# Kernel optimization log

Hardware: AMD Instinct MI355X
Metric: run time of the kernel (lower is better)

The kernel has to match this reference:

```python
import jax, jax.numpy as jnp
import numpy as np

# Hyperparameters (from init_kwargs)
B, N, K = 4, 16384, 16          # batch, points, kNN neighbors
C_IN, C_OUT = 64, 128           # in_planes, out_planes
KSIZE, DIL, STRIDE = 9, 1, 1    # WeightedConv1D kernel
PAD = DIL * (KSIZE // 2)        # padding = dilation*(k//2)
SIGMA = 0.02
NEG_SLOPE = 0.2                 # leakyrelu default in DeepGCN BasicConv
EPS = 1e-5                      # BatchNorm eps


def setup_inputs() -> dict:
    key = jax.random.key(0)
    ks = jax.random.split(key, 6)
    x = jax.random.normal(ks[0], (B, C_IN, N), jnp.float32)
    coords = jax.random.uniform(ks[1], (B, 3, N), jnp.float32)
    edge_index = jax.random.randint(ks[2], (2, B, N, K), 0, N)
    # EdgeConv MLP: Conv2d(2*C_IN, C_IN, 1, bias=False) -> BN -> LeakyReLU
    w_edge = jax.random.normal(ks[3], (C_IN, 2 * C_IN), jnp.float32) * (1.0 / np.sqrt(2 * C_IN))
    bn_gamma = jnp.ones((C_IN,), jnp.float32)
    bn_beta = jnp.zeros((C_IN,), jnp.float32)
    # WeightedConv1D learned kernel [C_out, C_in, k] + bias
    w_conv = jax.random.normal(ks[4], (C_OUT, C_IN, KSIZE), jnp.float32) * (1.0 / np.sqrt(C_IN * KSIZE))
    b_conv = jnp.zeros((C_OUT,), jnp.float32)
    return dict(x=x, coords=coords, edge_index=edge_index, w_edge=w_edge,
                bn_gamma=bn_gamma, bn_beta=bn_beta, w_conv=w_conv, b_conv=b_conv)


def _edge_conv(x, edge_index, w_edge, gamma, beta):
    # x: [B, C, N]; edge_index: [2, B, N, K]
    x_t = jnp.transpose(x, (0, 2, 1))                        # [B, N, C]
    gather = jax.vmap(lambda xt, idx: xt[idx])               # ([N,C],[N,K]) -> [N,K,C]
    x_j = gather(x_t, edge_index[0])                         # neighbor feats [B,N,K,C]
    x_i = gather(x_t, edge_index[1])                         # center feats   [B,N,K,C]
    feat = jnp.concatenate([x_i, x_j - x_i], axis=-1)        # [B,N,K,2C]
    h = jnp.einsum('bnkc,oc->bnko', feat, w_edge)            # 1x1 conv, bias=False
    # BatchNorm2d (training-mode batch stats over B,N,K per channel)
    mean = jnp.mean(h, axis=(0, 1, 2))
    var = jnp.var(h, axis=(0, 1, 2))
    h = (h - mean) * jax.lax.rsqrt(var + EPS) * gamma + beta
    h = jnp.where(h >= 0, h, NEG_SLOPE * h)                  # leaky_relu(0.2)
    return jnp.transpose(jnp.max(h, axis=2), (0, 2, 1))      # max over K -> [B,C,N]


def _weighted_conv(x, coords, w_conv, b_conv):
    # x: [B, C, N]; coords: [B, 3, N]
    xp = jnp.pad(x, ((0, 0), (0, 0), (PAD, PAD)))
    cp = jnp.pad(coords, ((0, 0), (0, 0), (PAD, PAD)))
    # unfold into k shifted views (k is small and static)
    x_win = jnp.stack([xp[:, :, j * DIL: j * DIL + N] for j in range(KSIZE)], axis=2)  # [B,C,k,N]
    c_win = jnp.stack([cp[:, :, j * DIL: j * DIL + N] for j in range(KSIZE)], axis=2)  # [B,3,k,N]
    d2 = jnp.sum((c_win - coords[:, :, None, :]) ** 2, axis=1)                          # [B,k,N]
    w = jnp.exp(-d2 / (SIGMA ** 2))                           # Gaussian coord weights
    out = jnp.einsum('bcjn,ocj->bon', x_win * w[:, None], w_conv)
    return out + b_conv[None, :, None]                        # [B, C_out, N]


def reference(x, coords, edge_index, w_edge, bn_gamma, bn_beta, w_conv, b_conv):
    h = _edge_conv(x, edge_index, w_edge, bn_gamma, bn_beta)
    return _weighted_conv(h, coords, w_conv, b_conv)
```

## Files before the change

kernel.cpp:

```cpp
#include <hip/hip_runtime.h>
#include <hip/hip_bf16.h>

#define B_ 4
#define N_ 16384
#define K_ 16
#define NEG 0.2f
#define EPSBN 1e-5f
#define INV_SIG2 2500.0f

typedef unsigned short u16;
typedef unsigned int   u32;
typedef __attribute__((ext_vector_type(8))) short short8;
typedef __attribute__((ext_vector_type(4))) float f32x4;

__device__ __forceinline__ float bf2f(u16 h){
  return __uint_as_float(((u32)h) << 16);
}
__device__ __forceinline__ u16 f2bf(float f){
  u32 x = __float_as_uint(f);
  x += 0x7fffu + ((x >> 16) & 1u);
  return (u16)(x >> 16);
}


__global__ void k0_wprep(const float* __restrict__ wconv, u16* __restrict__ wbf,
                         const float* __restrict__ we, u16* __restrict__ weA){
  const int idx = blockIdx.x * 256 + threadIdx.x;
  if (idx < 9*128*64){
    const int j = idx >> 13;
    const int rem = idx & 8191;
    const int o = rem >> 6, c = rem & 63;
    wbf[idx] = f2bf(wconv[(o*64 + c)*9 + j]);
  } else if (idx < 9*128*64 + 128*64){
    const int t = idx - 9*128*64;
    const int o = t >> 6, c = t & 63;
    float w;
    if (o < 64) w = we[o*128 + c] - we[o*128 + 64 + c];
    else        w = we[(o-64)*128 + 64 + c];
    weA[t] = f2bf(w);
  }
}

__global__ __launch_bounds__(256) void k1_uv(const float* __restrict__ x,
                                             const u16* __restrict__ weA,
                                             u16* __restrict__ uo,
                                             u16* __restrict__ vo){
  const int n0 = blockIdx.x * 64;
  const int b  = blockIdx.y;
  const int tid = threadIdx.x;
  const int w = tid >> 6, lane = tid & 63;
  const int r15 = lane & 15, kg = lane >> 4;

  __shared__ u16 tl[128*72];

  short8 a[2][2];
  #pragma unroll
  for (int of = 0; of < 2; ++of)
    #pragma unroll
    for (int kh = 0; kh < 2; ++kh)
      a[of][kh] = *(const short8*)&weA[(w*32 + of*16 + r15)*64 + kg*8 + kh*32];

  const float* xb = x + (size_t)b*64*N_ + n0 + r15;
  f32x4 acc[2][4];
  const f32x4 zero = {0.f, 0.f, 0.f, 0.f};

  #pragma unroll
  for (int nf = 0; nf < 4; ++nf){
    short8 bq[2];
    #pragma unroll
    for (int kh = 0; kh < 2; ++kh){
      float f[8];
      #pragma unroll
      for (int e = 0; e < 8; ++e)
        f[e] = xb[(size_t)(kg*8 + kh*32 + e)*N_ + nf*16];
      union { short8 s; u32 u[4]; } bb;
      #pragma unroll
      for (int e2 = 0; e2 < 4; ++e2)
        bb.u[e2] = (u32)f2bf(f[e2*2]) | ((u32)f2bf(f[e2*2+1]) << 16);
      bq[kh] = bb.s;
    }
    #pragma unroll
    for (int of = 0; of < 2; ++of){
      f32x4 p = __builtin_amdgcn_mfma_f32_16x16x32_bf16(a[of][0], bq[0], zero, 0, 0, 0);
      acc[of][nf] = __builtin_amdgcn_mfma_f32_16x16x32_bf16(a[of][1], bq[1], p, 0, 0, 0);
    }
  }

  #pragma unroll
  for (int of = 0; of < 2; ++of)
    #pragma unroll
    for (int rr = 0; rr < 4; ++rr){
      const int o = w*32 + of*16 + kg*4 + rr;
      #pragma unroll
      for (int nf = 0; nf < 4; ++nf)
        tl[o*72 + nf*16 + r15] = f2bf(acc[of][nf][rr]);
    }
  __syncthreads();

  const int arr = tid >> 7, half = (tid >> 6) & 1, n = tid & 63;
  const int ro = arr*64 + half*32;
  u32 pk[16];
  #pragma unroll
  for (int cc = 0; cc < 16; ++cc){
    const u16 lo = tl[(ro + cc*2    )*72 + n];
    const u16 hi = tl[(ro + cc*2 + 1)*72 + n];
    pk[cc] = (u32)lo | ((u32)hi << 16);
  }
  u16* dst = (arr ? vo : uo) + ((size_t)(half*B_ + b)*N_ + n0 + n)*32;
  *(uint4*)(dst +  0) = make_uint4(pk[0],  pk[1],  pk[2],  pk[3]);
  *(uint4*)(dst +  8) = make_uint4(pk[4],  pk[5],  pk[6],  pk[7]);
  *(uint4*)(dst + 16) = make_uint4(pk[8],  pk[9],  pk[10], pk[11]);
  *(uint4*)(dst + 24) = make_uint4(pk[12], pk[13], pk[14], pk[15]);
}

__global__ __launch_bounds__(256) void k2_gather(const u16* __restrict__ uo,
                                                 const u16* __restrict__ vo,
                                                 const int* __restrict__ eidx,
                                                 u16* __restrict__ wmaxo,
                                                 u16* __restrict__ wmino,
                                                 float* __restrict__ stats){
  const int bid = blockIdx.x;
  const int p8  = bid & 7;
  const int b   = p8 >> 1;
  const int h   = p8 & 1;
  const int n0  = (bid >> 3) * 32;
  const int tid = threadIdx.x;
  const int wid = tid >> 6, lane = tid & 63;
  const int kk = lane >> 4, cg = lane & 15;
  const int nb = n0 + wid*8;
  const size_t pbase = ((size_t)(h*B_ + b))*N_*32;
  const u16* ub = uo + pbase;
  const u16* vb = vo + pbase;

  __shared__ int eL[4][2][128];
  __shared__ float redS[4][32], redQ[4][32];

  const int* e0 = eidx + (b*N_ + nb)*K_;
  const int* e1 = eidx + B_*N_*K_ + (b*N_ + nb)*K_;
  if (lane < 32) *(int4*)&eL[wid][0][lane*4]      = *(const int4*)(e0 + lane*4);
  else           *(int4*)&eL[wid][1][(lane-32)*4] = *(const int4*)(e1 + (lane-32)*4);
  __syncthreads();

  float s0=0.f, s1=0.f, q0=0.f, q1=0.f;

  for (int p = 0; p < 8; ++p){
    int ji[4], ii[4];
    #pragma unroll
    for (int s = 0; s < 4; ++s){
      ji[s] = eL[wid][0][p*16 + s*4 + kk];
      ii[s] = eL[wid][1][p*16 + s*4 + kk];
    }
    u32 ua[4], va[4];
    #pragma unroll
    for (int s = 0; s < 4; ++s){
      ua[s] = *(const u32*)&ub[(size_t)ii[s]*32 + cg*2];
      va[s] = *(const u32*)&vb[(size_t)ji[s]*32 + cg*2];
    }
    float hL[4], hH[4];
    #pragma unroll
    for (int s = 0; s < 4; ++s){
      hL[s] = __uint_as_float(ua[s] << 16)         + __uint_as_float(va[s] << 16);
      hH[s] = __uint_as_float(ua[s] & 0xffff0000u) + __uint_as_float(va[s] & 0xffff0000u);
    }
    float mx0 = fmaxf(fmaxf(hL[0],hL[1]), fmaxf(hL[2],hL[3]));
    float mn0 = fminf(fminf(hL[0],hL[1]), fminf(hL[2],hL[3]));
    float mx1 = fmaxf(fmaxf(hH[0],hH[1]), fmaxf(hH[2],hH[3]));
    float mn1 = fminf(fminf(hH[0],hH[1]), fminf(hH[2],hH[3]));
    s0 += (hL[0]+hL[1]) + (hL[2]+hL[3]);
    s1 += (hH[0]+hH[1]) + (hH[2]+hH[3]);
    q0 = fmaf(hL[0],hL[0], fmaf(hL[1],hL[1], fmaf(hL[2],hL[2], fmaf(hL[3],hL[3], q0))));
    q1 = fmaf(hH[0],hH[0], fmaf(hH[1],hH[1], fmaf(hH[2],hH[2], fmaf(hH[3],hH[3], q1))));
    mx0 = fmaxf(mx0, __shfl_xor(mx0, 16)); mx0 = fmaxf(mx0, __shfl_xor(mx0, 32));
    mx1 = fmaxf(mx1, __shfl_xor(mx1, 16)); mx1 = fmaxf(mx1, __shfl_xor(mx1, 32));
    mn0 = fminf(mn0, __shfl_xor(mn0, 16)); mn0 = fminf(mn0, __shfl_xor(mn0, 32));
    mn1 = fminf(mn1, __shfl_xor(mn1, 16)); mn1 = fminf(mn1, __shfl_xor(mn1, 32));
    const int n = nb + p;
    if (lane < 16){
      const u32 pm = (u32)f2bf(mx0) | ((u32)f2bf(mx1) << 16);
      const u32 pn = (u32)f2bf(mn0) | ((u32)f2bf(mn1) << 16);
      *(u32*)&wmaxo[pbase + (size_t)n*32 + cg*2] = pm;
      *(u32*)&wmino[pbase + (size_t)n*32 + cg*2] = pn;
    }
  }

  s0 += __shfl_xor(s0,16); s0 += __shfl_xor(s0,32);
  s1 += __shfl_xor(s1,16); s1 += __shfl_xor(s1,32);
  q0 += __shfl_xor(q0,16); q0 += __shfl_xor(q0,32);
  q1 += __shfl_xor(q1,16); q1 += __shfl_xor(q1,32);
  if (lane < 16){
    redS[wid][cg*2]   = s0;  redS[wid][cg*2+1] = s1;
    redQ[wid][cg*2]   = q0;  redQ[wid][cg*2+1] = q1;
  }
  __syncthreads();
  if (tid < 32){
    atomicAdd(&stats[h*32 + tid], redS[0][tid]+redS[1][tid]+redS[2][tid]+redS[3][tid]);
  } else if (tid < 64){
    const int c = tid - 32;
    atomicAdd(&stats[64 + h*32 + c], redQ[0][c]+redQ[1][c]+redQ[2][c]+redQ[3][c]);
  }
}

__global__ __launch_bounds__(256) void k4_mfma(const u16* __restrict__ wmaxo,
                                               const u16* __restrict__ wmino,
                                               const float* __restrict__ stats,
                                               const float* __restrict__ gamma,
                                               const float* __restrict__ beta,
                                               const float* __restrict__ coords,
                                               const u16* __restrict__ wbf,
                                               const float* __restrict__ bconv,
                                               float* __restrict__ out){
  const int n0 = blockIdx.x * 64;
  const int b  = blockIdx.y;
  const int tid = threadIdx.x;
  const int w = tid >> 6, lane = tid & 63;
  const int r15 = lane & 15, kg = lane >> 4;

  __shared__ u16 hl[72*72];
  __shared__ float wgt[9*64];
  __shared__ float sctl[128];

  if (tid < 64){
    const float inv = 1.0f / (float)(B_*N_*K_);
    const float mean = stats[tid] * inv;
    const float var  = stats[64+tid] * inv - mean*mean;
    const float s = gamma[tid] * rsqrtf(var + EPSBN);
    sctl[tid] = s;
    sctl[64+tid] = beta[tid] - mean*s;
  }
  __syncthreads();

  {
    const int c = tid & 63;
    const float s = sctl[c], t = sctl[64+c];
    const u16* src = ((s >= 0.f) ? wmaxo : wmino)
                   + ((size_t)((c >> 5)*B_ + b))*N_*32 + (c & 31);
    #pragma unroll
    for (int it = 0; it < 18; ++it){
      const int ml = (tid >> 6) + it*4;
      const int m = n0 - 4 + ml;
      float hv = 0.f;
      if (m >= 0 && m < N_){
        hv = fmaf(s, bf2f(src[(size_t)m*32]), t);
        hv = (hv >= 0.f) ? hv : NEG*hv;
      }
      hl[ml*72 + c] = f2bf(hv);
    }
  }
  for (int idx = tid; idx < 576; idx += 256){
    const int j = idx >> 6, n = idx & 63;
    const int mc = n0 + n, mt = mc + j - 4;
    float wv = 0.f;
    if (mt >= 0 && mt < N_){
      float d2 = 0.f;
      #pragma unroll
      for (int d = 0; d < 3; ++d){
        const float dd = coords[(b*3+d)*N_ + mt] - coords[(b*3+d)*N_ + mc];
        d2 = fmaf(dd, dd, d2);
      }
      wv = __expf(-INV_SIG2 * d2);
    }
    wgt[idx] = wv;
  }
  __syncthreads();

  const u16* abase = wbf + ((w*32 + r15)*64 + kg*8);
  const u16* hbase = &hl[r15*72 + kg*8];
  f32x4 acc[2][4] = {};
  const f32x4 zero = {0.f, 0.f, 0.f, 0.f};

  for (int j = 0; j < 9; ++j){
    float wj[4];
    #pragma unroll
    for (int nf = 0; nf < 4; ++nf) wj[nf] = wgt[j*64 + nf*16 + r15];
    short8 bfr[4][2];
    #pragma unroll
    for (int nf = 0; nf < 4; ++nf){
      bfr[nf][0] = *(const short8*)&hbase[(nf*16 + j)*72];
      bfr[nf][1] = *(const short8*)&hbase[(nf*16 + j)*72 + 32];
    }
    #pragma unroll
    for (int of = 0; of < 2; ++of){
      const short8 a0 = *(const short8*)&abase[j*8192 + of*1024];
      const short8 a1 = *(const short8*)&abase[j*8192 + of*1024 + 32];
      #pragma unroll
      for (int nf = 0; nf < 4; ++nf){
        f32x4 p = __builtin_amdgcn_mfma_f32_16x16x32_bf16(a0, bfr[nf][0], zero, 0, 0, 0);
        p = __builtin_amdgcn_mfma_f32_16x16x32_bf16(a1, bfr[nf][1], p, 0, 0, 0);
        #pragma unroll
        for (int r = 0; r < 4; ++r)
          acc[of][nf][r] = fmaf(wj[nf], p[r], acc[of][nf][r]);
      }
    }
  }

  #pragma unroll
  for (int of = 0; of < 2; ++of){
    #pragma unroll
    for (int r = 0; r < 4; ++r){
      const int o = w*32 + of*16 + kg*4 + r;
      const float bs = bconv[o];
      float* dst = &out[(size_t)(b*128 + o)*N_ + n0 + r15];
      #pragma unroll
      for (int nf = 0; nf < 4; ++nf)
        dst[nf*16] = acc[of][nf][r] + bs;
    }
  }
}

extern "C" void kernel_launch(void* const* d_in, const int* in_sizes, int n_in,
                              void* d_out, int out_size, void* d_ws, size_t ws_size,
                              hipStream_t stream){
  const float* x      = (const float*)d_in[0];
  const float* coords = (const float*)d_in[1];
  const int*   eidx   = (const int*)  d_in[2];
  const float* we     = (const float*)d_in[3];
  const float* gamma  = (const float*)d_in[4];
  const float* beta   = (const float*)d_in[5];
  const float* wconv  = (const float*)d_in[6];
  const float* bconv  = (const float*)d_in[7];
  float* out = (float*)d_out;
  char* ws = (char*)d_ws;
  u16* u     = (u16*)(ws);
  u16* v     = (u16*)(ws + 8388608);
  u16* wmax_ = (u16*)(ws + 16777216);
  u16* wmin_ = (u16*)(ws + 25165824);
  float* stats = (float*)(ws + 33554432);
  u16* wbf     = (u16*)(ws + 33555456);
  u16* weA     = (u16*)(ws + 33555456 + 147456);

  hipMemsetAsync(stats, 0, 512, stream);
  k0_wprep<<<320, 256, 0, stream>>>(wconv, wbf, we, weA);
  k1_uv<<<dim3(N_/64, B_), 256, 0, stream>>>(x, weA, u, v);
  k2_gather<<<4096, 256, 0, stream>>>(u, v, eidx, wmax_, wmin_, stats);
  k4_mfma<<<dim3(N_/64, B_), 256, 0, stream>>>(wmax_, wmin_, stats, gamma, beta,
                                               coords, wbf, bconv, out);
}
```

Baseline: 125.7 us.

## Halve k4 point tile, swizzle LDS halo layout, fold stats memset into k0

Shrinks the k4 point tile from 64 to 32 points per block, doubling the grid and setting a 6-blocks-per-CU launch bound to raise occupancy. The LDS halo tile becomes an XOR-free rotated (swizzled) 64-wide layout to avoid bank conflicts without padding, read back with two 8-byte loads per fragment. It also zeroes the BN stats buffer inside the weight-prep kernel instead of issuing a separate memset. The cost is more halo overhead (40 rows per 32 points) and less weight reuse per block.

New measurement: 133.6 us. 1.06x slower.

```diff
diff --git a/kernel.cpp b/kernel.cpp
--- a/kernel.cpp
+++ b/kernel.cpp
@@ -24,8 +24,10 @@
 
 
 __global__ void k0_wprep(const float* __restrict__ wconv, u16* __restrict__ wbf,
-                         const float* __restrict__ we, u16* __restrict__ weA){
+                         const float* __restrict__ we, u16* __restrict__ weA,
+                         float* __restrict__ stats){
   const int idx = blockIdx.x * 256 + threadIdx.x;
+  if (idx < 128) stats[idx] = 0.f;
   if (idx < 9*128*64){
     const int j = idx >> 13;
     const int rem = idx & 8191;
@@ -200,23 +202,23 @@
   }
 }
 
-__global__ __launch_bounds__(256) void k4_mfma(const u16* __restrict__ wmaxo,
-                                               const u16* __restrict__ wmino,
-                                               const float* __restrict__ stats,
-                                               const float* __restrict__ gamma,
-                                               const float* __restrict__ beta,
-                                               const float* __restrict__ coords,
-                                               const u16* __restrict__ wbf,
-                                               const float* __restrict__ bconv,
-                                               float* __restrict__ out){
-  const int n0 = blockIdx.x * 64;
+__global__ __launch_bounds__(256, 6) void k4_mfma(const u16* __restrict__ wmaxo,
+                                                  const u16* __restrict__ wmino,
+                                                  const float* __restrict__ stats,
+                                                  const float* __restrict__ gamma,
+                                                  const float* __restrict__ beta,
+                                                  const float* __restrict__ coords,
+                                                  const u16* __restrict__ wbf,
+                                                  const float* __restrict__ bconv,
+                                                  float* __restrict__ out){
+  const int n0 = blockIdx.x * 32;
   const int b  = blockIdx.y;
   const int tid = threadIdx.x;
   const int w = tid >> 6, lane = tid & 63;
   const int r15 = lane & 15, kg = lane >> 4;
 
-  __shared__ u16 hl[72*72];
-  __shared__ float wgt[9*64];
+  __shared__ __align__(16) u16 hl[40*64];
+  __shared__ float wgt[9*32];
   __shared__ float sctl[128];
 
   if (tid < 64){
@@ -229,25 +231,21 @@
   }
   __syncthreads();
 
-  {
-    const int c = tid & 63;
-    const float s = sctl[c], t = sctl[64+c];
-    const u16* src = ((s >= 0.f) ? wmaxo : wmino)
-                   + ((size_t)((c >> 5)*B_ + b))*N_*32 + (c & 31);
-    #pragma unroll
-    for (int it = 0; it < 18; ++it){
-      const int ml = (tid >> 6) + it*4;
-      const int m = n0 - 4 + ml;
-      float hv = 0.f;
-      if (m >= 0 && m < N_){
-        hv = fmaf(s, bf2f(src[(size_t)m*32]), t);
-        hv = (hv >= 0.f) ? hv : NEG*hv;
-      }
-      hl[ml*72 + c] = f2bf(hv);
-    }
-  }
-  for (int idx = tid; idx < 576; idx += 256){
-    const int j = idx >> 6, n = idx & 63;
+  for (int idx = tid; idx < 40*64; idx += 256){
+    const int ml = idx >> 6, c = idx & 63;
+    const int m = n0 - 4 + ml;
+    float hv = 0.f;
+    if (m >= 0 && m < N_){
+      const float s = sctl[c], t = sctl[64+c];
+      const u16 g = ((s >= 0.f) ? wmaxo : wmino)
+                    [((size_t)((c>>5)*B_ + b))*N_*32 + (size_t)m*32 + (c&31)];
+      hv = fmaf(s, bf2f(g), t);
+      hv = fmaxf(hv, NEG*hv);
+    }
+    hl[ml*64 + ((c + 4*ml) & 63)] = f2bf(hv);
+  }
+  for (int idx = tid; idx < 288; idx += 256){
+    const int j = idx >> 5, n = idx & 31;
     const int mc = n0 + n, mt = mc + j - 4;
     float wv = 0.f;
     if (mt >= 0 && mt < N_){
@@ -264,31 +262,39 @@
   __syncthreads();
 
   const u16* abase = wbf + ((w*32 + r15)*64 + kg*8);
-  const u16* hbase = &hl[r15*72 + kg*8];
-  f32x4 acc[2][4] = {};
+  f32x4 acc[2][2] = {};
   const f32x4 zero = {0.f, 0.f, 0.f, 0.f};
 
   for (int j = 0; j < 9; ++j){
-    float wj[4];
-    #pragma unroll
-    for (int nf = 0; nf < 4; ++nf) wj[nf] = wgt[j*64 + nf*16 + r15];
-    short8 bfr[4][2];
-    #pragma unroll
-    for (int nf = 0; nf < 4; ++nf){
-      bfr[nf][0] = *(const short8*)&hbase[(nf*16 + j)*72];
-      bfr[nf][1] = *(const short8*)&hbase[(nf*16 + j)*72 + 32];
+    const float wj0 = wgt[j*32 + r15];
+    const float wj1 = wgt[j*32 + 16 + r15];
+    short8 bfr[2][2];
+    #pragma unroll
+    for (int nf = 0; nf < 2; ++nf){
+      const int row = r15 + nf*16 + j;
+      const int rb = row*64, r4 = row*4;
+      #pragma unroll
+      for (int kh = 0; kh < 2; ++kh){
+        const int cb = kg*8 + kh*32;
+        const uint2 g0 = *(const uint2*)&hl[rb + ((cb     + r4) & 63)];
+        const uint2 g1 = *(const uint2*)&hl[rb + ((cb + 4 + r4) & 63)];
+        union { short8 s; u32 u[4]; } bb;
+        bb.u[0] = g0.x; bb.u[1] = g0.y; bb.u[2] = g1.x; bb.u[3] = g1.y;
+        bfr[nf][kh] = bb.s;
+      }
     }
     #pragma unroll
     for (int of = 0; of < 2; ++of){
       const short8 a0 = *(const short8*)&abase[j*8192 + of*1024];
       const short8 a1 = *(const short8*)&abase[j*8192 + of*1024 + 32];
       #pragma unroll
-      for (int nf = 0; nf < 4; ++nf){
+      for (int nf = 0; nf < 2; ++nf){
         f32x4 p = __builtin_amdgcn_mfma_f32_16x16x32_bf16(a0, bfr[nf][0], zero, 0, 0, 0);
         p = __builtin_amdgcn_mfma_f32_16x16x32_bf16(a1, bfr[nf][1], p, 0, 0, 0);
+        const float wj = nf ? wj1 : wj0;
         #pragma unroll
         for (int r = 0; r < 4; ++r)
-          acc[of][nf][r] = fmaf(wj[nf], p[r], acc[of][nf][r]);
+          acc[of][nf][r] = fmaf(wj, p[r], acc[of][nf][r]);
       }
     }
   }
@@ -301,7 +307,7 @@
       const float bs = bconv[o];
       float* dst = &out[(size_t)(b*128 + o)*N_ + n0 + r15];
       #pragma unroll
-      for (int nf = 0; nf < 4; ++nf)
+      for (int nf = 0; nf < 2; ++nf)
         dst[nf*16] = acc[of][nf][r] + bs;
     }
   }
@@ -328,10 +334,9 @@
   u16* wbf     = (u16*)(ws + 33555456);
   u16* weA     = (u16*)(ws + 33555456 + 147456);
 
-  hipMemsetAsync(stats, 0, 512, stream);
-  k0_wprep<<<320, 256, 0, stream>>>(wconv, wbf, we, weA);
+  k0_wprep<<<320, 256, 0, stream>>>(wconv, wbf, we, weA, stats);
   k1_uv<<<dim3(N_/64, B_), 256, 0, stream>>>(x, weA, u, v);
   k2_gather<<<4096, 256, 0, stream>>>(u, v, eidx, wmax_, wmin_, stats);
-  k4_mfma<<<dim3(N_/64, B_), 256, 0, stream>>>(wmax_, wmin_, stats, gamma, beta,
+  k4_mfma<<<dim3(N_/32, B_), 256, 0, stream>>>(wmax_, wmin_, stats, gamma, beta,
                                                coords, wbf, bconv, out);
 }
```
